# Kernel tuning notes

Measured on AMD Instinct MI355X. Metric: run time of the kernel, lower is better.

The kernel has to match this reference:

```python
import jax, jax.numpy as jnp
import numpy as np

D_MODEL = 1024
N_HEAD = 16
HEAD_DIM = D_MODEL // N_HEAD
B, S = 4, 2048


def setup_inputs() -> dict:
    key = jax.random.key(0)
    ks = jax.random.split(key, 11)
    scale = 1.0 / np.sqrt(D_MODEL)
    inp = {
        "q": jax.random.normal(ks[0], (B, S, D_MODEL), jnp.float32),
        "k": jax.random.normal(ks[1], (B, S, D_MODEL), jnp.float32),
        "v": jax.random.normal(ks[2], (B, S, D_MODEL), jnp.float32),
        # torch nn.Linear weights: [out_features, in_features], y = x @ W.T + b
        "Wq": jax.random.normal(ks[3], (D_MODEL, D_MODEL), jnp.float32) * scale,
        "bq": jax.random.normal(ks[4], (D_MODEL,), jnp.float32) * scale,
        "Wk": jax.random.normal(ks[5], (D_MODEL, D_MODEL), jnp.float32) * scale,
        "bk": jax.random.normal(ks[6], (D_MODEL,), jnp.float32) * scale,
        "Wv": jax.random.normal(ks[7], (D_MODEL, D_MODEL), jnp.float32) * scale,
        "bv": jax.random.normal(ks[8], (D_MODEL,), jnp.float32) * scale,
        "Wo": jax.random.normal(ks[9], (D_MODEL, D_MODEL), jnp.float32) * scale,
        "bo": jax.random.normal(ks[10], (D_MODEL,), jnp.float32) * scale,
    }
    return inp


def _split_heads(x):
    # [B, S, D] -> [B, H, S, hd]
    b, s, _ = x.shape
    return x.reshape(b, s, N_HEAD, HEAD_DIM).transpose(0, 2, 1, 3)


def reference(q, k, v, Wq, bq, Wk, bk, Wv, bv, Wo, bo):
    qh = _split_heads(q @ Wq.T + bq)
    kh = _split_heads(k @ Wk.T + bk)
    vh = _split_heads(v @ Wv.T + bv)
    scores = jnp.einsum("bhqd,bhkd->bhqk", qh, kh) / jnp.sqrt(
        jnp.asarray(HEAD_DIM, qh.dtype)
    )
    weights = jax.nn.softmax(scores, axis=-1)  # [B, H, Sq, Sk]
    ctx = jnp.einsum("bhqk,bhkd->bhqd", weights, vh)
    b, h, s, d = ctx.shape
    ctx = ctx.transpose(0, 2, 1, 3).reshape(b, s, h * d)  # [B, S, D]
    return ctx @ Wo.T + bo
```

## Files before the change

### kernel.cpp

```cpp
#include <hip/hip_runtime.h>
#include <hip/hip_bf16.h>

typedef float   f32x4   __attribute__((ext_vector_type(4)));
typedef __bf16  bf16x8  __attribute__((ext_vector_type(8)));
typedef unsigned short u16x8 __attribute__((ext_vector_type(8)));
typedef unsigned short u16x4 __attribute__((ext_vector_type(4)));

#define DEVI __device__ __forceinline__

DEVI unsigned short f2bf_bits(float f) {
    __bf16 h = (__bf16)f;
    return __builtin_bit_cast(unsigned short, h);
}

DEVI f32x4 mfma_bf16(bf16x8 a, bf16x8 b, f32x4 c) {
    return __builtin_amdgcn_mfma_f32_16x16x32_bf16(a, b, c, 0, 0, 0);
}

DEVI float fast_exp2(float x) {
#if __has_builtin(__builtin_amdgcn_exp2f)
    return __builtin_amdgcn_exp2f(x);
#else
    float r;
    asm("v_exp_f32 %0, %1" : "=v"(r) : "v"(x));
    return r;
#endif
}

DEVI void gload16(const void* g, void* l) {
    __builtin_amdgcn_global_load_lds(
        (const __attribute__((address_space(1))) void*)g,
        (__attribute__((address_space(3))) void*)l, 16, 0, 0);
}

__global__ __launch_bounds__(256) void convert_w_kernel(
    const float* __restrict__ Wq, const float* __restrict__ Wk,
    const float* __restrict__ Wv, unsigned short* __restrict__ Wb)
{
    int idx = blockIdx.x * 256 + threadIdx.x;
    int which = idx >> 17;
    int off = (idx & 131071) * 8;
    const float* src = which == 0 ? Wq : (which == 1 ? Wk : Wv);
    f32x4 a = *(const f32x4*)(src + off);
    f32x4 b = *(const f32x4*)(src + off + 4);
    u16x8 h;
#pragma unroll
    for (int j = 0; j < 4; ++j) { h[j] = f2bf_bits(a[j]); h[4 + j] = f2bf_bits(b[j]); }
    *(u16x8*)(Wb + (size_t)which * 1048576 + off) = h;
}

__global__ __launch_bounds__(256) void convert_wo_kernel(
    const float* __restrict__ Wo, unsigned short* __restrict__ Wb)
{
    int off = (blockIdx.x * 256 + threadIdx.x) * 8;
    f32x4 a = *(const f32x4*)(Wo + off);
    f32x4 b = *(const f32x4*)(Wo + off + 4);
    u16x8 h;
#pragma unroll
    for (int j = 0; j < 4; ++j) { h[j] = f2bf_bits(a[j]); h[4 + j] = f2bf_bits(b[j]); }
    *(u16x8*)(Wb + off) = h;
}

__global__ __launch_bounds__(256) void proj_gemm_kernel(
    const float* __restrict__ Ap, const unsigned short* __restrict__ Wb,
    const float* __restrict__ bias, unsigned short* __restrict__ Cp,
    int M, int N, int K, float scale)
{
    __shared__ __align__(16) char ldsA[128 * 128];
    __shared__ __align__(16) char ldsB[128 * 128];
    const int t = threadIdx.x;
    const int wave = t >> 6, lane = t & 63;
    const int g = lane >> 4, c = lane & 15;
    const int rowbase = blockIdx.x * 128;
    const int colbase = blockIdx.y * 128;
    const int wr = (wave >> 1) * 64, wc = (wave & 1) * 64;

    const int arow = lane >> 3;
    const int aslot = (lane & 7) ^ arow;

    const float* fbase[4];
#pragma unroll
    for (int ch = 0; ch < 4; ++ch) {
        int id = ch * 256 + t;
        int row = id >> 3;
        int col = (id & 7) * 8;
        fbase[ch] = Ap + (size_t)(rowbase + row) * K + col;
    }

    f32x4 pre0[4], pre1[4];
#pragma unroll
    for (int ch = 0; ch < 4; ++ch) {
        pre0[ch] = *(const f32x4*)(fbase[ch]);
        pre1[ch] = *(const f32x4*)(fbase[ch] + 4);
    }

    f32x4 acc[4][4] = {};

    for (int kt = 0; kt < K; kt += 64) {
#pragma unroll
        for (int j = 0; j < 4; ++j) {
            int rg = wave * 4 + j;
            int row = rg * 8 + arow;
            gload16(Wb + (size_t)(colbase + row) * K + kt + aslot * 8,
                    ldsB + rg * 1024);
        }

#pragma unroll
        for (int ch = 0; ch < 4; ++ch) {
            int id = ch * 256 + t;
            int row = id >> 3;
            int col = (id & 7) * 8;
            int dst = row * 128 + ((col * 2) ^ ((row & 7) << 4));
            u16x8 hv;
#pragma unroll
            for (int j = 0; j < 4; ++j) { hv[j] = f2bf_bits(pre0[ch][j]); hv[4 + j] = f2bf_bits(pre1[ch][j]); }
            *(u16x8*)(ldsA + dst) = hv;
        }
        __syncthreads();

        if (kt + 64 < K) {
#pragma unroll
            for (int ch = 0; ch < 4; ++ch) {
                pre0[ch] = *(const f32x4*)(fbase[ch] + kt + 64);
                pre1[ch] = *(const f32x4*)(fbase[ch] + kt + 68);
            }
        }

#pragma unroll
        for (int kk = 0; kk < 2; ++kk) {
            bf16x8 af[4], bfr[4];
#pragma unroll
            for (int i = 0; i < 4; ++i) {
                int ra = wr + i * 16 + c;
                af[i] = *(const bf16x8*)(ldsA + ra * 128 + ((kk * 64 + g * 16) ^ ((ra & 7) << 4)));
                int rb = wc + i * 16 + c;
                bfr[i] = *(const bf16x8*)(ldsB + rb * 128 + ((kk * 64 + g * 16) ^ ((rb & 7) << 4)));
            }
#pragma unroll
            for (int i = 0; i < 4; ++i)
#pragma unroll
                for (int j = 0; j < 4; ++j)
                    acc[i][j] = mfma_bf16(af[i], bfr[j], acc[i][j]);
        }
        __syncthreads();
    }

#pragma unroll
    for (int j = 0; j < 4; ++j) {
        int coln = colbase + wc + j * 16 + c;
        float bv = bias[coln];
#pragma unroll
        for (int i = 0; i < 4; ++i) {
            int row0 = rowbase + wr + i * 16 + g * 4;
#pragma unroll
            for (int r = 0; r < 4; ++r) {
                float val = (acc[i][j][r] + bv) * scale;
                Cp[(size_t)(row0 + r) * N + coln] = f2bf_bits(val);
            }
        }
    }
}

__global__ __launch_bounds__(256) void out_gemm_kernel(
    const unsigned short* __restrict__ Ab, const unsigned short* __restrict__ Wb,
    const float* __restrict__ bias, float* __restrict__ Cp,
    int M, int N, int K)
{
    __shared__ __align__(16) char ldsA[128 * 128];
    __shared__ __align__(16) char ldsB[128 * 128];
    const int t = threadIdx.x;
    const int wave = t >> 6, lane = t & 63;
    const int g = lane >> 4, c = lane & 15;
    const int rowbase = blockIdx.x * 128;
    const int colbase = blockIdx.y * 128;
    const int wr = (wave >> 1) * 64, wc = (wave & 1) * 64;

    const int arow = lane >> 3;
    const int aslot = (lane & 7) ^ arow;

    f32x4 acc[4][4] = {};

    for (int kt = 0; kt < K; kt += 64) {
#pragma unroll
        for (int j = 0; j < 4; ++j) {
            int rg = wave * 4 + j;
            int row = rg * 8 + arow;
            gload16(Ab + (size_t)(rowbase + row) * K + kt + aslot * 8,
                    ldsA + rg * 1024);
            gload16(Wb + (size_t)(colbase + row) * K + kt + aslot * 8,
                    ldsB + rg * 1024);
        }
        __syncthreads();

#pragma unroll
        for (int kk = 0; kk < 2; ++kk) {
            bf16x8 af[4], bfr[4];
#pragma unroll
            for (int i = 0; i < 4; ++i) {
                int ra = wr + i * 16 + c;
                af[i] = *(const bf16x8*)(ldsA + ra * 128 + ((kk * 64 + g * 16) ^ ((ra & 7) << 4)));
                int rb = wc + i * 16 + c;
                bfr[i] = *(const bf16x8*)(ldsB + rb * 128 + ((kk * 64 + g * 16) ^ ((rb & 7) << 4)));
            }
#pragma unroll
            for (int i = 0; i < 4; ++i)
#pragma unroll
                for (int j = 0; j < 4; ++j)
                    acc[i][j] = mfma_bf16(af[i], bfr[j], acc[i][j]);
        }
        __syncthreads();
    }

#pragma unroll
    for (int j = 0; j < 4; ++j) {
        int coln = colbase + wc + j * 16 + c;
        float bv = bias[coln];
#pragma unroll
        for (int i = 0; i < 4; ++i) {
            int row0 = rowbase + wr + i * 16 + g * 4;
#pragma unroll
            for (int r = 0; r < 4; ++r)
                Cp[(size_t)(row0 + r) * N + coln] = acc[i][j][r] + bv;
        }
    }
}

__global__ __launch_bounds__(256) void transpose_v_kernel(
    const unsigned short* __restrict__ Vp, unsigned short* __restrict__ Vt)
{
    __shared__ unsigned short tile[64][72];
    const int t = threadIdx.x;
    const int bh = blockIdx.y, b = bh >> 4, h = bh & 15;
    const int s0 = blockIdx.x * 64;
#pragma unroll
    for (int ch = 0; ch < 2; ++ch) {
        int id = ch * 256 + t;
        int srow = id >> 3, dcol = (id & 7) * 8;
        u16x8 v = *(const u16x8*)(Vp + (size_t)(b * 2048 + s0 + srow) * 1024 + h * 64 + dcol);
        *(u16x8*)&tile[srow][dcol] = v;
    }
    __syncthreads();
#pragma unroll
    for (int ch = 0; ch < 2; ++ch) {
        int id = ch * 256 + t;
        int drow = id >> 3, scol = (id & 7) * 8;
        u16x8 ov;
#pragma unroll
        for (int j = 0; j < 8; ++j) ov[j] = tile[scol + j][drow];
        *(u16x8*)(Vt + (size_t)(bh * 64 + drow) * 2048 + s0 + scol) = ov;
    }
}

__global__ __launch_bounds__(256) void attn_kernel(
    const unsigned short* __restrict__ Qp, const unsigned short* __restrict__ Kp,
    const unsigned short* __restrict__ Vt, unsigned short* __restrict__ ctx)
{
    __shared__ __align__(16) char ldsK[64 * 128];
    __shared__ __align__(16) char ldsV[64 * 128];
    __shared__ __align__(16) char ldsP[4][2][16 * 128];
    const int t = threadIdx.x;
    const int wave = t >> 6, lane = t & 63;
    const int g = lane >> 4, c = lane & 15;

    const int d = blockIdx.x;
    const int slot = d >> 3;
    const int bh = (d & 7) * 8 + (slot >> 4);
    const int qblk = slot & 15;
    const int b = bh >> 4, h = bh & 15;
    const int qb = qblk * 128;

    bf16x8 qf0[2], qf1[2];
    {
        const unsigned short* q0 = Qp + (size_t)(b * 2048 + qb + wave * 32 + c) * 1024 + h * 64;
        qf0[0] = *(const bf16x8*)(q0 + 8 * g);
        qf0[1] = *(const bf16x8*)(q0 + 32 + 8 * g);
        const unsigned short* q1 = q0 + (size_t)16 * 1024;
        qf1[0] = *(const bf16x8*)(q1 + 8 * g);
        qf1[1] = *(const bf16x8*)(q1 + 32 + 8 * g);
    }

    f32x4 o0[4] = {}, o1[4] = {};
    float psum0 = 0.f, psum1 = 0.f;

    const int row0 = t >> 3, colB = (t & 7) * 8;
    const int row1 = 32 + row0;
    const int dst0 = row0 * 128 + ((colB * 2) ^ ((row0 & 7) << 4));
    const int dst1 = row1 * 128 + ((colB * 2) ^ ((row1 & 7) << 4));
    const unsigned short* Ksrc = Kp + (size_t)(b * 2048) * 1024 + h * 64;
    const unsigned short* Vsrc = Vt + (size_t)(bh * 64) * 2048;

    u16x8 kv0 = *(const u16x8*)(Ksrc + (size_t)row0 * 1024 + colB);
    u16x8 kv1 = *(const u16x8*)(Ksrc + (size_t)row1 * 1024 + colB);
    u16x8 vv0 = *(const u16x8*)(Vsrc + (size_t)row0 * 2048 + colB);
    u16x8 vv1 = *(const u16x8*)(Vsrc + (size_t)row1 * 2048 + colB);

    char* pw0 = ldsP[wave][0];
    char* pw1 = ldsP[wave][1];

    for (int kb = 0; kb < 2048; kb += 64) {
        *(u16x8*)(ldsK + dst0) = kv0;
        *(u16x8*)(ldsK + dst1) = kv1;
        *(u16x8*)(ldsV + dst0) = vv0;
        *(u16x8*)(ldsV + dst1) = vv1;
        __syncthreads();

        if (kb + 64 < 2048) {
            kv0 = *(const u16x8*)(Ksrc + (size_t)(kb + 64 + row0) * 1024 + colB);
            kv1 = *(const u16x8*)(Ksrc + (size_t)(kb + 64 + row1) * 1024 + colB);
            vv0 = *(const u16x8*)(Vsrc + (size_t)row0 * 2048 + kb + 64 + colB);
            vv1 = *(const u16x8*)(Vsrc + (size_t)row1 * 2048 + kb + 64 + colB);
        }

        f32x4 s0[4] = {}, s1[4] = {};
#pragma unroll
        for (int kk = 0; kk < 2; ++kk) {
            bf16x8 kf[4];
#pragma unroll
            for (int ti = 0; ti < 4; ++ti) {
                int rk = ti * 16 + c;
                kf[ti] = *(const bf16x8*)(ldsK + rk * 128 + ((kk * 64 + g * 16) ^ ((rk & 7) << 4)));
            }
#pragma unroll
            for (int ti = 0; ti < 4; ++ti) {
                s0[ti] = mfma_bf16(kf[ti], qf0[kk], s0[ti]);
                s1[ti] = mfma_bf16(kf[ti], qf1[kk], s1[ti]);
            }
        }

#pragma unroll
        for (int ti = 0; ti < 4; ++ti) {
            float p0 = fast_exp2(s0[ti][0]);
            float p1 = fast_exp2(s0[ti][1]);
            float p2 = fast_exp2(s0[ti][2]);
            float p3 = fast_exp2(s0[ti][3]);
            psum0 += (p0 + p1) + (p2 + p3);
            u16x4 hp;
            hp[0] = f2bf_bits(p0); hp[1] = f2bf_bits(p1);
            hp[2] = f2bf_bits(p2); hp[3] = f2bf_bits(p3);
            *(u16x4*)(pw0 + c * 128 + ((ti * 32 + g * 8) ^ ((c & 7) << 4))) = hp;
        }
#pragma unroll
        for (int ti = 0; ti < 4; ++ti) {
            float p0 = fast_exp2(s1[ti][0]);
            float p1 = fast_exp2(s1[ti][1]);
            float p2 = fast_exp2(s1[ti][2]);
            float p3 = fast_exp2(s1[ti][3]);
            psum1 += (p0 + p1) + (p2 + p3);
            u16x4 hp;
            hp[0] = f2bf_bits(p0); hp[1] = f2bf_bits(p1);
            hp[2] = f2bf_bits(p2); hp[3] = f2bf_bits(p3);
            *(u16x4*)(pw1 + c * 128 + ((ti * 32 + g * 8) ^ ((c & 7) << 4))) = hp;
        }

#pragma unroll
        for (int kk = 0; kk < 2; ++kk) {
            bf16x8 vf[4];
#pragma unroll
            for (int ti = 0; ti < 4; ++ti) {
                int rv = ti * 16 + c;
                vf[ti] = *(const bf16x8*)(ldsV + rv * 128 + ((kk * 64 + g * 16) ^ ((rv & 7) << 4)));
            }
            bf16x8 pa0 = *(const bf16x8*)(pw0 + c * 128 + ((kk * 64 + g * 16) ^ ((c & 7) << 4)));
            bf16x8 pa1 = *(const bf16x8*)(pw1 + c * 128 + ((kk * 64 + g * 16) ^ ((c & 7) << 4)));
#pragma unroll
            for (int ti = 0; ti < 4; ++ti) {
                o0[ti] = mfma_bf16(pa0, vf[ti], o0[ti]);
                o1[ti] = mfma_bf16(pa1, vf[ti], o1[ti]);
            }
        }
        __syncthreads();
    }

    psum0 += __shfl_xor(psum0, 16);
    psum0 += __shfl_xor(psum0, 32);
    psum1 += __shfl_xor(psum1, 16);
    psum1 += __shfl_xor(psum1, 32);

#pragma unroll
    for (int r = 0; r < 4; ++r) {
        float inv0 = 1.0f / __shfl(psum0, 4 * g + r);
        float inv1 = 1.0f / __shfl(psum1, 4 * g + r);
        int row0q = qb + wave * 32 + 4 * g + r;
        int row1q = row0q + 16;
#pragma unroll
        for (int ti = 0; ti < 4; ++ti) {
            int col = h * 64 + ti * 16 + c;
            ctx[(size_t)(b * 2048 + row0q) * 1024 + col] = f2bf_bits(o0[ti][r] * inv0);
            ctx[(size_t)(b * 2048 + row1q) * 1024 + col] = f2bf_bits(o1[ti][r] * inv1);
        }
    }
}

extern "C" void kernel_launch(void* const* d_in, const int* in_sizes, int n_in,
                              void* d_out, int out_size, void* d_ws, size_t ws_size,
                              hipStream_t stream)
{
    const float* q  = (const float*)d_in[0];
    const float* k  = (const float*)d_in[1];
    const float* v  = (const float*)d_in[2];
    const float* Wq = (const float*)d_in[3];
    const float* bq = (const float*)d_in[4];
    const float* Wk = (const float*)d_in[5];
    const float* bk = (const float*)d_in[6];
    const float* Wv = (const float*)d_in[7];
    const float* bv = (const float*)d_in[8];
    const float* Wo = (const float*)d_in[9];
    const float* bo = (const float*)d_in[10];
    float* out = (float*)d_out;

    char* ws = (char*)d_ws;
    const size_t SZ = (size_t)8192 * 1024 * 2;
    unsigned short* Qp = (unsigned short*)(ws);
    unsigned short* Kp = (unsigned short*)(ws + SZ);
    unsigned short* Vp = (unsigned short*)(ws + 2 * SZ);
    unsigned short* Vt = (unsigned short*)(ws + 3 * SZ);
    unsigned short* ctx = Vp;
    unsigned short* Wbf = Vt;
    unsigned short* Wob = Kp;

    const float QSCALE = 0.1803368801111244f;

    convert_w_kernel<<<dim3(1536), 256, 0, stream>>>(Wq, Wk, Wv, Wbf);

    dim3 gg(64, 8);
    proj_gemm_kernel<<<gg, 256, 0, stream>>>(q, Wbf,           bq, Qp, 8192, 1024, 1024, QSCALE);
    proj_gemm_kernel<<<gg, 256, 0, stream>>>(k, Wbf + 1048576, bk, Kp, 8192, 1024, 1024, 1.0f);
    proj_gemm_kernel<<<gg, 256, 0, stream>>>(v, Wbf + 2097152, bv, Vp, 8192, 1024, 1024, 1.0f);
    transpose_v_kernel<<<dim3(32, 64), 256, 0, stream>>>(Vp, Vt);
    attn_kernel<<<dim3(1024), 256, 0, stream>>>(Qp, Kp, Vt, ctx);
    convert_wo_kernel<<<dim3(512), 256, 0, stream>>>(Wo, Wob);
    out_gemm_kernel<<<gg, 256, 0, stream>>>(ctx, Wob, bo, out, 8192, 1024, 1024);
}
```

Measured before the change: 219.7 us.

## Split attention KV loop across two half-blocks and merge partials in LDS

The attention kernel now launches 512 threads per block. Each 256-thread half processes half of the key/value sequence with its own LDS tiles. Partial outputs and softmax sums from the second half are written to LDS, added by the first half, normalized and stored. This doubles the waves working on each query tile to shorten the serial KV loop, at the cost of 64KB LDS per block, an extra reduction step, and possibly lower block occupancy.

```diff
diff --git a/kernel.cpp b/kernel.cpp
--- a/kernel.cpp
+++ b/kernel.cpp
@@ -251,15 +251,17 @@
     }
 }
 
-__global__ __launch_bounds__(256) void attn_kernel(
+__global__ __launch_bounds__(512) void attn_kernel(
     const unsigned short* __restrict__ Qp, const unsigned short* __restrict__ Kp,
     const unsigned short* __restrict__ Vt, unsigned short* __restrict__ ctx)
 {
-    __shared__ __align__(16) char ldsK[64 * 128];
-    __shared__ __align__(16) char ldsV[64 * 128];
-    __shared__ __align__(16) char ldsP[4][2][16 * 128];
-    const int t = threadIdx.x;
-    const int wave = t >> 6, lane = t & 63;
+    __shared__ __align__(16) char ldsBuf[65536];
+    const int t512 = threadIdx.x;
+    const int wave = t512 >> 6;
+    const int hf = wave >> 2;
+    const int wp = wave & 3;
+    const int t = t512 & 255;
+    const int lane = t512 & 63;
     const int g = lane >> 4, c = lane & 15;
 
     const int d = blockIdx.x;
@@ -269,9 +271,14 @@
     const int b = bh >> 4, h = bh & 15;
     const int qb = qblk * 128;
 
+    char* ldsK = ldsBuf + hf * 8192;
+    char* ldsV = ldsBuf + 16384 + hf * 8192;
+    char* pw0 = ldsBuf + 32768 + wave * 4096;
+    char* pw1 = pw0 + 2048;
+
     bf16x8 qf0[2], qf1[2];
     {
-        const unsigned short* q0 = Qp + (size_t)(b * 2048 + qb + wave * 32 + c) * 1024 + h * 64;
+        const unsigned short* q0 = Qp + (size_t)(b * 2048 + qb + wp * 32 + c) * 1024 + h * 64;
         qf0[0] = *(const bf16x8*)(q0 + 8 * g);
         qf0[1] = *(const bf16x8*)(q0 + 32 + 8 * g);
         const unsigned short* q1 = q0 + (size_t)16 * 1024;
@@ -286,29 +293,27 @@
     const int row1 = 32 + row0;
     const int dst0 = row0 * 128 + ((colB * 2) ^ ((row0 & 7) << 4));
     const int dst1 = row1 * 128 + ((colB * 2) ^ ((row1 & 7) << 4));
+    const int koff = hf * 1024;
     const unsigned short* Ksrc = Kp + (size_t)(b * 2048) * 1024 + h * 64;
     const unsigned short* Vsrc = Vt + (size_t)(bh * 64) * 2048;
 
-    u16x8 kv0 = *(const u16x8*)(Ksrc + (size_t)row0 * 1024 + colB);
-    u16x8 kv1 = *(const u16x8*)(Ksrc + (size_t)row1 * 1024 + colB);
-    u16x8 vv0 = *(const u16x8*)(Vsrc + (size_t)row0 * 2048 + colB);
-    u16x8 vv1 = *(const u16x8*)(Vsrc + (size_t)row1 * 2048 + colB);
-
-    char* pw0 = ldsP[wave][0];
-    char* pw1 = ldsP[wave][1];
-
-    for (int kb = 0; kb < 2048; kb += 64) {
+    u16x8 kv0 = *(const u16x8*)(Ksrc + (size_t)(koff + row0) * 1024 + colB);
+    u16x8 kv1 = *(const u16x8*)(Ksrc + (size_t)(koff + row1) * 1024 + colB);
+    u16x8 vv0 = *(const u16x8*)(Vsrc + (size_t)row0 * 2048 + koff + colB);
+    u16x8 vv1 = *(const u16x8*)(Vsrc + (size_t)row1 * 2048 + koff + colB);
+
+    for (int kb = 0; kb < 1024; kb += 64) {
         *(u16x8*)(ldsK + dst0) = kv0;
         *(u16x8*)(ldsK + dst1) = kv1;
         *(u16x8*)(ldsV + dst0) = vv0;
         *(u16x8*)(ldsV + dst1) = vv1;
         __syncthreads();
 
-        if (kb + 64 < 2048) {
-            kv0 = *(const u16x8*)(Ksrc + (size_t)(kb + 64 + row0) * 1024 + colB);
-            kv1 = *(const u16x8*)(Ksrc + (size_t)(kb + 64 + row1) * 1024 + colB);
-            vv0 = *(const u16x8*)(Vsrc + (size_t)row0 * 2048 + kb + 64 + colB);
-            vv1 = *(const u16x8*)(Vsrc + (size_t)row1 * 2048 + kb + 64 + colB);
+        if (kb + 64 < 1024) {
+            kv0 = *(const u16x8*)(Ksrc + (size_t)(koff + kb + 64 + row0) * 1024 + colB);
+            kv1 = *(const u16x8*)(Ksrc + (size_t)(koff + kb + 64 + row1) * 1024 + colB);
+            vv0 = *(const u16x8*)(Vsrc + (size_t)row0 * 2048 + koff + kb + 64 + colB);
+            vv1 = *(const u16x8*)(Vsrc + (size_t)row1 * 2048 + koff + kb + 64 + colB);
         }
 
         f32x4 s0[4] = {}, s1[4] = {};
@@ -376,17 +381,43 @@
     psum1 += __shfl_xor(psum1, 16);
     psum1 += __shfl_xor(psum1, 32);
 
-#pragma unroll
-    for (int r = 0; r < 4; ++r) {
-        float inv0 = 1.0f / __shfl(psum0, 4 * g + r);
-        float inv1 = 1.0f / __shfl(psum1, 4 * g + r);
-        int row0q = qb + wave * 32 + 4 * g + r;
-        int row1q = row0q + 16;
-#pragma unroll
-        for (int ti = 0; ti < 4; ++ti) {
-            int col = h * 64 + ti * 16 + c;
-            ctx[(size_t)(b * 2048 + row0q) * 1024 + col] = f2bf_bits(o0[ti][r] * inv0);
-            ctx[(size_t)(b * 2048 + row1q) * 1024 + col] = f2bf_bits(o1[ti][r] * inv1);
+    if (hf == 1) {
+        f32x4* ex = (f32x4*)ldsBuf;
+#pragma unroll
+        for (int i = 0; i < 4; ++i) {
+            ex[i * 256 + wp * 64 + lane] = o0[i];
+            ex[(4 + i) * 256 + wp * 64 + lane] = o1[i];
+        }
+        float* ps = (float*)(ldsBuf + 32768) + (wp * 64 + lane) * 2;
+        ps[0] = psum0;
+        ps[1] = psum1;
+    }
+    __syncthreads();
+    if (hf == 0) {
+        f32x4* ex = (f32x4*)ldsBuf;
+#pragma unroll
+        for (int i = 0; i < 4; ++i) {
+            f32x4 a = ex[i * 256 + wp * 64 + lane];
+            f32x4 b2 = ex[(4 + i) * 256 + wp * 64 + lane];
+            o0[i] += a;
+            o1[i] += b2;
+        }
+        float* ps = (float*)(ldsBuf + 32768) + (wp * 64 + lane) * 2;
+        psum0 += ps[0];
+        psum1 += ps[1];
+
+#pragma unroll
+        for (int r = 0; r < 4; ++r) {
+            float inv0 = 1.0f / __shfl(psum0, 4 * g + r);
+            float inv1 = 1.0f / __shfl(psum1, 4 * g + r);
+            int row0q = qb + wp * 32 + 4 * g + r;
+            int row1q = row0q + 16;
+#pragma unroll
+            for (int ti = 0; ti < 4; ++ti) {
+                int col = h * 64 + ti * 16 + c;
+                ctx[(size_t)(b * 2048 + row0q) * 1024 + col] = f2bf_bits(o0[ti][r] * inv0);
+                ctx[(size_t)(b * 2048 + row1q) * 1024 + col] = f2bf_bits(o1[ti][r] * inv1);
+            }
         }
     }
 }
@@ -427,7 +458,7 @@
     proj_gemm_kernel<<<gg, 256, 0, stream>>>(k, Wbf + 1048576, bk, Kp, 8192, 1024, 1024, 1.0f);
     proj_gemm_kernel<<<gg, 256, 0, stream>>>(v, Wbf + 2097152, bv, Vp, 8192, 1024, 1024, 1.0f);
     transpose_v_kernel<<<dim3(32, 64), 256, 0, stream>>>(Vp, Vt);
-    attn_kernel<<<dim3(1024), 256, 0, stream>>>(Qp, Kp, Vt, ctx);
+    attn_kernel<<<dim3(1024), 512, 0, stream>>>(Qp, Kp, Vt, ctx);
     convert_wo_kernel<<<dim3(512), 256, 0, stream>>>(Wo, Wob);
     out_gemm_kernel<<<gg, 256, 0, stream>>>(ctx, Wob, bo, out, 8192, 1024, 1024);
 }
```

Result: no change. 220.2 us (+0.2%).

## Double-buffer K/V tiles in LDS with two-ahead register prefetch

Applied to the files above, without the earlier changes.

K and V shared-memory tiles become double-buffered. The next tile is written to the alternate buffer while the current one is consumed, and global loads are issued two tiles ahead. This removes one barrier per iteration and overlaps LDS stores and global latency with MFMA work. LDS usage per block doubles for K/V, which may reduce occupancy.

```diff
diff --git a/kernel.cpp b/kernel.cpp
--- a/kernel.cpp
+++ b/kernel.cpp
@@ -255,8 +255,8 @@
     const unsigned short* __restrict__ Qp, const unsigned short* __restrict__ Kp,
     const unsigned short* __restrict__ Vt, unsigned short* __restrict__ ctx)
 {
-    __shared__ __align__(16) char ldsK[64 * 128];
-    __shared__ __align__(16) char ldsV[64 * 128];
+    __shared__ __align__(16) char ldsK[2][64 * 128];
+    __shared__ __align__(16) char ldsV[2][64 * 128];
     __shared__ __align__(16) char ldsP[4][2][16 * 128];
     const int t = threadIdx.x;
     const int wave = t >> 6, lane = t & 63;
@@ -289,26 +289,42 @@
     const unsigned short* Ksrc = Kp + (size_t)(b * 2048) * 1024 + h * 64;
     const unsigned short* Vsrc = Vt + (size_t)(bh * 64) * 2048;
 
+    char* pw0 = ldsP[wave][0];
+    char* pw1 = ldsP[wave][1];
+
     u16x8 kv0 = *(const u16x8*)(Ksrc + (size_t)row0 * 1024 + colB);
     u16x8 kv1 = *(const u16x8*)(Ksrc + (size_t)row1 * 1024 + colB);
     u16x8 vv0 = *(const u16x8*)(Vsrc + (size_t)row0 * 2048 + colB);
     u16x8 vv1 = *(const u16x8*)(Vsrc + (size_t)row1 * 2048 + colB);
-
-    char* pw0 = ldsP[wave][0];
-    char* pw1 = ldsP[wave][1];
-
-    for (int kb = 0; kb < 2048; kb += 64) {
-        *(u16x8*)(ldsK + dst0) = kv0;
-        *(u16x8*)(ldsK + dst1) = kv1;
-        *(u16x8*)(ldsV + dst0) = vv0;
-        *(u16x8*)(ldsV + dst1) = vv1;
-        __syncthreads();
-
-        if (kb + 64 < 2048) {
-            kv0 = *(const u16x8*)(Ksrc + (size_t)(kb + 64 + row0) * 1024 + colB);
-            kv1 = *(const u16x8*)(Ksrc + (size_t)(kb + 64 + row1) * 1024 + colB);
-            vv0 = *(const u16x8*)(Vsrc + (size_t)row0 * 2048 + kb + 64 + colB);
-            vv1 = *(const u16x8*)(Vsrc + (size_t)row1 * 2048 + kb + 64 + colB);
+    *(u16x8*)(ldsK[0] + dst0) = kv0;
+    *(u16x8*)(ldsK[0] + dst1) = kv1;
+    *(u16x8*)(ldsV[0] + dst0) = vv0;
+    *(u16x8*)(ldsV[0] + dst1) = vv1;
+    kv0 = *(const u16x8*)(Ksrc + (size_t)(64 + row0) * 1024 + colB);
+    kv1 = *(const u16x8*)(Ksrc + (size_t)(64 + row1) * 1024 + colB);
+    vv0 = *(const u16x8*)(Vsrc + (size_t)row0 * 2048 + 64 + colB);
+    vv1 = *(const u16x8*)(Vsrc + (size_t)row1 * 2048 + 64 + colB);
+    __syncthreads();
+
+    for (int i = 0; i < 32; ++i) {
+        const int cur = i & 1;
+        char* kbuf = ldsK[cur];
+        char* vbuf = ldsV[cur];
+
+        if (i + 1 < 32) {
+            char* kn = ldsK[cur ^ 1];
+            char* vn = ldsV[cur ^ 1];
+            *(u16x8*)(kn + dst0) = kv0;
+            *(u16x8*)(kn + dst1) = kv1;
+            *(u16x8*)(vn + dst0) = vv0;
+            *(u16x8*)(vn + dst1) = vv1;
+        }
+        if (i + 2 < 32) {
+            int kb2 = (i + 2) * 64;
+            kv0 = *(const u16x8*)(Ksrc + (size_t)(kb2 + row0) * 1024 + colB);
+            kv1 = *(const u16x8*)(Ksrc + (size_t)(kb2 + row1) * 1024 + colB);
+            vv0 = *(const u16x8*)(Vsrc + (size_t)row0 * 2048 + kb2 + colB);
+            vv1 = *(const u16x8*)(Vsrc + (size_t)row1 * 2048 + kb2 + colB);
         }
 
         f32x4 s0[4] = {}, s1[4] = {};
@@ -318,7 +334,7 @@
 #pragma unroll
             for (int ti = 0; ti < 4; ++ti) {
                 int rk = ti * 16 + c;
-                kf[ti] = *(const bf16x8*)(ldsK + rk * 128 + ((kk * 64 + g * 16) ^ ((rk & 7) << 4)));
+                kf[ti] = *(const bf16x8*)(kbuf + rk * 128 + ((kk * 64 + g * 16) ^ ((rk & 7) << 4)));
             }
 #pragma unroll
             for (int ti = 0; ti < 4; ++ti) {
@@ -358,7 +374,7 @@
 #pragma unroll
             for (int ti = 0; ti < 4; ++ti) {
                 int rv = ti * 16 + c;
-                vf[ti] = *(const bf16x8*)(ldsV + rv * 128 + ((kk * 64 + g * 16) ^ ((rv & 7) << 4)));
+                vf[ti] = *(const bf16x8*)(vbuf + rv * 128 + ((kk * 64 + g * 16) ^ ((rv & 7) << 4)));
             }
             bf16x8 pa0 = *(const bf16x8*)(pw0 + c * 128 + ((kk * 64 + g * 16) ^ ((c & 7) << 4)));
             bf16x8 pa1 = *(const bf16x8*)(pw1 + c * 128 + ((kk * 64 + g * 16) ^ ((c & 7) << 4)));
```

Result: slower. 229.4 us (+4.4%).
